# Kernel tuning notes

Hardware: AMD Instinct MI355X
Metric: run time of the kernel (lower is better)

The kernel has to match this reference:

```python
import jax, jax.numpy as jnp
import numpy as np

BN_EPS = 1e-5


def setup_inputs() -> dict:
    key = jax.random.key(0)
    ks = jax.random.split(key, 12)
    B, N, S, D1, D2 = 8, 8192, 2048, 128, 256
    C_in = D2 + D1  # 384
    mlp = [256, 128]
    inp = {
        "xyz1": jax.random.normal(ks[0], (B, 3, N), jnp.float32),
        "xyz2": jax.random.normal(ks[1], (B, 3, S), jnp.float32),
        "points1": jax.random.normal(ks[2], (B, D1, N), jnp.float32),
        "points2": jax.random.normal(ks[3], (B, D2, S), jnp.float32),
    }
    # conv0: in 384 -> 256, conv1: 256 -> 128 (1x1 Conv1d == per-point matmul)
    inp["w0"] = jax.random.normal(ks[4], (mlp[0], C_in), jnp.float32) * (1.0 / np.sqrt(C_in))
    inp["b0"] = jax.random.normal(ks[5], (mlp[0],), jnp.float32) * 0.01
    inp["g0"] = jnp.ones((mlp[0],), jnp.float32)
    inp["be0"] = jnp.zeros((mlp[0],), jnp.float32)
    inp["w1"] = jax.random.normal(ks[6], (mlp[1], mlp[0]), jnp.float32) * (1.0 / np.sqrt(mlp[0]))
    inp["b1"] = jax.random.normal(ks[7], (mlp[1],), jnp.float32) * 0.01
    inp["g1"] = jnp.ones((mlp[1],), jnp.float32)
    inp["be1"] = jnp.zeros((mlp[1],), jnp.float32)
    return inp


def _conv_bn_relu(x, w, b, g, be):
    # 1x1 Conv1d + BatchNorm1d (training-mode batch stats, biased var) + ReLU
    x = jnp.einsum("oc,bcn->bon", w, x) + b[None, :, None]
    m = jnp.mean(x, axis=(0, 2), keepdims=True)
    v = jnp.var(x, axis=(0, 2), keepdims=True)
    x = (x - m) * jax.lax.rsqrt(v + BN_EPS) * g[None, :, None] + be[None, :, None]
    return jax.nn.relu(x)


def reference(xyz1, xyz2, points1, points2, w0, b0, g0, be0, w1, b1, g1, be1):
    B, _, N = xyz1.shape
    S = xyz2.shape[2]
    src = jnp.transpose(xyz1, (0, 2, 1))  # [B,N,3]
    dst = jnp.transpose(xyz2, (0, 2, 1))  # [B,S,3]
    # squared pairwise distance [B,N,S]
    dist = (
        jnp.sum(src * src, axis=-1)[:, :, None]
        + jnp.sum(dst * dst, axis=-1)[:, None, :]
        - 2.0 * jnp.einsum("bnc,bsc->bns", src, dst)
    )
    # 3 nearest neighbors (smallest dist, sorted)
    neg_d, idx = jax.lax.top_k(-dist, 3)  # [B,N,3]
    d3 = -neg_d
    recip = 1.0 / (d3 + 1e-8)
    weight = recip / jnp.sum(recip, axis=-1, keepdims=True)  # [B,N,3]
    p2t = jnp.transpose(points2, (0, 2, 1))  # [B,S,D']
    gathered = jnp.take_along_axis(
        p2t, idx.reshape(B, N * 3)[:, :, None], axis=1
    ).reshape(B, N, 3, -1)  # [B,N,3,D']
    interp = jnp.einsum("bnkd,bnk->bdn", gathered, weight)  # [B,D',N]
    x = jnp.concatenate([interp, points1], axis=1)  # [B,D'+D,N]
    x = _conv_bn_relu(x, w0, b0, g0, be0)
    x = _conv_bn_relu(x, w1, b1, g1, be1)
    return x
```

## Files before the change

### kernel.cpp

```cpp
#include <hip/hip_runtime.h>
#include <hip/hip_bf16.h>

constexpr int kB = 8, kN = 8192, kS = 2048;
constexpr int kD1 = 128, kD2 = 256, kCin = 384, kM0 = 256, kM1 = 128;
constexpr float kEps = 1e-5f;
constexpr int kReps = 64;

typedef float f32x4 __attribute__((ext_vector_type(4)));
typedef short bf16x8 __attribute__((ext_vector_type(8)));
typedef unsigned short u16x4 __attribute__((ext_vector_type(4)));

__device__ inline unsigned short f2bf(float f) {
    __hip_bfloat16 h = __float2bfloat16(f);
    return *reinterpret_cast<unsigned short*>(&h);
}
__device__ inline float bf2f(unsigned short u) {
    unsigned int v = (unsigned int)u << 16;
    return *reinterpret_cast<float*>(&v);
}
__device__ inline unsigned uminu(unsigned a, unsigned b) { return a < b ? a : b; }
__device__ inline unsigned med3u(unsigned a, unsigned b, unsigned c) {
    unsigned d;
    asm("v_med3_u32 %0, %1, %2, %3" : "=v"(d) : "v"(a), "v"(b), "v"(c));
    return d;
}
#define INS4(K0, K1, K2, K3, X) do { unsigned _x = (X);          \
    K3 = med3u(_x, K2, K3);                                      \
    K2 = med3u(_x, K1, K2);                                      \
    K1 = med3u(_x, K0, K1);                                      \
    K0 = uminu(_x, K0); } while (0)

__global__ __launch_bounds__(256) void prep_kernel(
    const float* __restrict__ points2, float* __restrict__ p2t,
    const float* __restrict__ points1, unsigned short* __restrict__ xt,
    const float* __restrict__ xyz2, f32x4* __restrict__ spk,
    float* __restrict__ repl, float* __restrict__ smallstats,
    const float* __restrict__ w0, unsigned short* __restrict__ w0bf,
    const float* __restrict__ w1, unsigned short* __restrict__ w1bf)
{
    __shared__ float tl[64][69];
    const int bx = blockIdx.x;
    const int t = threadIdx.x;
    const int rlo = t >> 4, rhi = t & 15;
    if (bx < 1024) {
        const int b = bx >> 7, tile = bx & 127;
        const int s0 = (tile & 31) * 64, c0 = (tile >> 5) * 64;
#pragma unroll
        for (int r = 0; r < 4; ++r) {
            const int cl = rlo + r * 16;
            f32x4 v = *(const f32x4*)(points2 + ((size_t)(b * kD2 + c0 + cl)) * kS + s0 + rhi * 4);
#pragma unroll
            for (int j = 0; j < 4; ++j) tl[cl][rhi * 4 + j] = v[j];
        }
        __syncthreads();
#pragma unroll
        for (int r = 0; r < 4; ++r) {
            const int sl = rlo + r * 16;
            f32x4 v;
#pragma unroll
            for (int j = 0; j < 4; ++j) v[j] = tl[rhi * 4 + j][sl];
            *(f32x4*)(p2t + ((size_t)(b * kS + s0 + sl)) * kD2 + c0 + rhi * 4) = v;
        }
    } else if (bx < 3072) {
        const int idx = bx - 1024;
        const int b = idx >> 8, tile = idx & 255;
        const int n0 = (tile & 127) * 64, c0 = (tile >> 7) * 64;
#pragma unroll
        for (int r = 0; r < 4; ++r) {
            const int cl = rlo + r * 16;
            f32x4 v = *(const f32x4*)(points1 + ((size_t)(b * kD1 + c0 + cl)) * kN + n0 + rhi * 4);
#pragma unroll
            for (int j = 0; j < 4; ++j) tl[cl][rhi * 4 + j] = v[j];
        }
        __syncthreads();
#pragma unroll
        for (int r = 0; r < 4; ++r) {
            const int nl = rlo + r * 16;
            u16x4 u;
#pragma unroll
            for (int j = 0; j < 4; ++j) u[j] = f2bf(tl[rhi * 4 + j][nl]);
            *(u16x4*)(xt + ((size_t)(b * kN + n0 + nl)) * kCin + 256 + c0 + rhi * 4) = u;
        }
    } else if (bx < 3080) {
        const int b = bx - 3072;
        const float* x2 = xyz2 + b * 3 * kS;
        for (int s = t; s < kS; s += 256) {
            float sx = x2[s], sy = x2[kS + s], sz = x2[2 * kS + s];
            f32x4 q = {sx, sy, sz, fmaf(sx, sx, fmaf(sy, sy, sz * sz))};
            spk[b * kS + s] = q;
        }
        for (int i = b * 6144 + t; i < (b + 1) * 6144; i += 256) repl[i] = 0.f;
        if (b == 0) for (int i = t; i < 772; i += 256) smallstats[i] = 0.f;
    } else if (bx < 3096) {
        const int base = (bx - 3080) * 256 + t;
        for (int c = base; c < kM0 * kCin / 4; c += 4096) {
            f32x4 v = *(const f32x4*)(w0 + (size_t)c * 4);
            u16x4 u = {f2bf(v[0]), f2bf(v[1]), f2bf(v[2]), f2bf(v[3])};
            *(u16x4*)(w0bf + (size_t)c * 4) = u;
        }
    } else {
        const int base = (bx - 3096) * 256 + t;
        for (int c = base; c < kM1 * kM0 / 4; c += 2048) {
            f32x4 v = *(const f32x4*)(w1 + (size_t)c * 4);
            u16x4 u = {f2bf(v[0]), f2bf(v[1]), f2bf(v[2]), f2bf(v[3])};
            *(u16x4*)(w1bf + (size_t)c * 4) = u;
        }
    }
}

__global__ __launch_bounds__(256) void knn_interp_kernel(
    const float* __restrict__ xyz1, const f32x4* __restrict__ spk,
    const float* __restrict__ p2t, unsigned short* __restrict__ xt,
    int* __restrict__ flaglist, int* __restrict__ flagcount)
{
    __shared__ f32x4 sp[kS];
    const int bb = blockIdx.x >> 7;
    const int nblk = (blockIdx.x & 127) << 6;
    const int t = threadIdx.x;
    for (int s = t; s < kS; s += 256) sp[s] = spk[bb * kS + s];
    __syncthreads();
    const int q = t >> 2, c = t & 3;
    const int nq = nblk + q;
    const float* x1 = xyz1 + bb * 3 * kN;
    const float px = x1[nq], py = x1[kN + nq], pz = x1[2 * kN + nq];
    const float ax = -2.f * px, ay = -2.f * py, az = -2.f * pz;
    const float pp = fmaf(px, px, fmaf(py, py, pz * pz));

    unsigned k0 = 0xFFFFFFFFu, k1 = 0xFFFFFFFFu, k2 = 0xFFFFFFFFu, k3 = 0xFFFFFFFFu;
#pragma unroll 8
    for (int i = 0; i < 512; ++i) {
        const f32x4 qv = sp[4 * i + c];
        const float e = fmaxf(fmaf(ax, qv[0], fmaf(ay, qv[1], fmaf(az, qv[2], qv[3] + pp))), 0.f);
        const unsigned x = (__float_as_uint(e) & 0xFFFFF800u) | (unsigned)(4 * i + c);
        INS4(k0, k1, k2, k3, x);
    }
#pragma unroll
    for (int off = 1; off <= 2; off <<= 1) {
        const unsigned m0 = __shfl_xor(k0, off), m1 = __shfl_xor(k1, off);
        const unsigned m2 = __shfl_xor(k2, off), m3 = __shfl_xor(k3, off);
        INS4(k0, k1, k2, k3, m0); INS4(k0, k1, k2, k3, m1);
        INS4(k0, k1, k2, k3, m2); INS4(k0, k1, k2, k3, m3);
    }

    bool flag = false;
    float w0f = 0.f, w1f = 0.f, w2f = 0.f;
    int i0 = (int)(k0 & 2047u), i1 = (int)(k1 & 2047u), i2 = (int)(k2 & 2047u);
    if (c == 0) {
        const float v2t = __uint_as_float(k2 & 0xFFFFF800u);
        const float v3t = __uint_as_float(k3 & 0xFFFFF800u);
        flag = (v3t - v2t) <= fmaf(v3t, 1e-3f, 2.5e-4f);
        const double dpx = (double)px, dpy = (double)py, dpz = (double)pz;
        const f32x4 s0 = sp[i0], s1 = sp[i1], s2 = sp[i2];
        double d0 = (dpx - s0[0]) * (dpx - s0[0]) + (dpy - s0[1]) * (dpy - s0[1]) + (dpz - s0[2]) * (dpz - s0[2]);
        double d1 = (dpx - s1[0]) * (dpx - s1[0]) + (dpy - s1[1]) * (dpy - s1[1]) + (dpz - s1[2]) * (dpz - s1[2]);
        double d2 = (dpx - s2[0]) * (dpx - s2[0]) + (dpy - s2[1]) * (dpy - s2[1]) + (dpz - s2[2]) * (dpz - s2[2]);
        if (d1 < d0 || (d1 == d0 && i1 < i0)) { double td = d0; d0 = d1; d1 = td; int ti = i0; i0 = i1; i1 = ti; }
        if (d2 < d1 || (d2 == d1 && i2 < i1)) { double td = d1; d1 = d2; d2 = td; int ti = i1; i1 = i2; i2 = ti; }
        if (d1 < d0 || (d1 == d0 && i1 < i0)) { double td = d0; d0 = d1; d1 = td; int ti = i0; i0 = i1; i1 = ti; }
        const double r0 = 1.0 / (d0 + 1e-8), r1 = 1.0 / (d1 + 1e-8), r2 = 1.0 / (d2 + 1e-8);
        const double rs = 1.0 / (r0 + r1 + r2);
        w0f = (float)(r0 * rs); w1f = (float)(r1 * rs); w2f = (float)(r2 * rs);
    }
    const int src = (t & 63) & ~3;
    w0f = __shfl(w0f, src); w1f = __shfl(w1f, src); w2f = __shfl(w2f, src);
    i0 = __shfl(i0, src); i1 = __shfl(i1, src); i2 = __shfl(i2, src);

    {
        const unsigned long long bal = __ballot(flag);
        if (bal) {
            const int l = t & 63;
            int base = 0;
            if (l == 0) base = atomicAdd(flagcount, __popcll(bal));
            base = __shfl(base, 0);
            if (flag) {
                const int pre = __popcll(bal & ((1ull << l) - 1ull));
                flaglist[base + pre] = (bb << 13) | nq;
            }
        }
    }

    const f32x4* row0 = (const f32x4*)(p2t + ((size_t)(bb * kS) + i0) * kD2);
    const f32x4* row1 = (const f32x4*)(p2t + ((size_t)(bb * kS) + i1) * kD2);
    const f32x4* row2 = (const f32x4*)(p2t + ((size_t)(bb * kS) + i2) * kD2);
    unsigned short* dst = xt + ((size_t)(bb * kN) + nq) * kCin;
#pragma unroll 4
    for (int j = 0; j < 16; ++j) {
        const int ch = c + 4 * j;
        f32x4 v = w0f * row0[ch] + w1f * row1[ch] + w2f * row2[ch];
        u16x4 u = {f2bf(v[0]), f2bf(v[1]), f2bf(v[2]), f2bf(v[3])};
        *(u16x4*)(dst + ch * 4) = u;
    }
}
#undef INS4

__global__ __launch_bounds__(256) void knn_fallback_kernel(
    const float* __restrict__ xyz1, const f32x4* __restrict__ spk,
    const float* __restrict__ p2t, unsigned short* __restrict__ xt,
    const int* __restrict__ flaglist, const int* __restrict__ flagcount)
{
    const int cnt = *flagcount;
    const int t = threadIdx.x;
    const int w = t >> 6, l = t & 63;
    for (int idx = blockIdx.x * 4 + w; idx < cnt; idx += gridDim.x * 4) {
        const int code = flaglist[idx];
        const int b = code >> 13, n = code & 8191;
        const float* x1 = xyz1 + b * 3 * kN;
        const double px = (double)x1[n], py = (double)x1[kN + n], pz = (double)x1[2 * kN + n];
        double d0 = 1e300, d1 = 1e300, d2 = 1e300;
        int i0 = 0, i1 = 0, i2 = 0;
        for (int s = l; s < kS; s += 64) {
            const f32x4 q = spk[b * kS + s];
            const double ex = px - (double)q[0], ey = py - (double)q[1], ez = pz - (double)q[2];
            const double d = ex * ex + ey * ey + ez * ez;
            if (d < d2) {
                if (d < d1) {
                    if (d < d0) { d2 = d1; i2 = i1; d1 = d0; i1 = i0; d0 = d; i0 = s; }
                    else        { d2 = d1; i2 = i1; d1 = d;  i1 = s; }
                } else          { d2 = d;  i2 = s; }
            }
        }
#pragma unroll
        for (int off = 1; off < 64; off <<= 1) {
            double pd0 = __shfl_xor(d0, off), pd1 = __shfl_xor(d1, off), pd2 = __shfl_xor(d2, off);
            int pi0 = __shfl_xor(i0, off), pi1 = __shfl_xor(i1, off), pi2 = __shfl_xor(i2, off);
#pragma unroll
            for (int m = 0; m < 3; ++m) {
                const double pd = (m == 0) ? pd0 : (m == 1) ? pd1 : pd2;
                const int pi = (m == 0) ? pi0 : (m == 1) ? pi1 : pi2;
                if (pd < d2 || (pd == d2 && pi < i2)) {
                    if (pd < d1 || (pd == d1 && pi < i1)) {
                        if (pd < d0 || (pd == d0 && pi < i0)) {
                            d2 = d1; i2 = i1; d1 = d0; i1 = i0; d0 = pd; i0 = pi;
                        } else { d2 = d1; i2 = i1; d1 = pd; i1 = pi; }
                    } else { d2 = pd; i2 = pi; }
                }
            }
        }
        const double r0 = 1.0 / (d0 + 1e-8), r1 = 1.0 / (d1 + 1e-8), r2 = 1.0 / (d2 + 1e-8);
        const double rs = 1.0 / (r0 + r1 + r2);
        const float w0f = (float)(r0 * rs), w1f = (float)(r1 * rs), w2f = (float)(r2 * rs);
        const f32x4* row0 = (const f32x4*)(p2t + ((size_t)(b * kS) + i0) * kD2);
        const f32x4* row1 = (const f32x4*)(p2t + ((size_t)(b * kS) + i1) * kD2);
        const f32x4* row2 = (const f32x4*)(p2t + ((size_t)(b * kS) + i2) * kD2);
        const f32x4 v = w0f * row0[l] + w1f * row1[l] + w2f * row2[l];
        u16x4 u = {f2bf(v[0]), f2bf(v[1]), f2bf(v[2]), f2bf(v[3])};
        *(u16x4*)(xt + ((size_t)(b * kN) + n) * kCin + l * 4) = u;
    }
}

__device__ inline int swz(int row, int ks) {
    return row * 32 + ((ks ^ ((row >> 1) & 3)) << 3);
}

template <int K, int MTOT, bool BNRELU, int OUTMODE, bool STATS>
__global__ __launch_bounds__(256) void gemm_bn_kernel(
    const unsigned short* __restrict__ Wbf, const unsigned short* __restrict__ X,
    const float* __restrict__ scale, const float* __restrict__ shift,
    unsigned short* __restrict__ Yb, float* __restrict__ Yf,
    float* __restrict__ repl)
{
    constexpr int BM = 128, BN = 64;
    __shared__ unsigned short Al[2][BM * 32], Bl[2][BN * 32];
    __shared__ float ssum[BM], ssq[BM];
    __shared__ float s_sc[K], s_sh[K];
    const int t = threadIdx.x;
    const int bn = blockIdx.x * BN, bo = blockIdx.y * BM, b = blockIdx.z;
    const int l = t & 63, w = t >> 6;
    const int wm = (w >> 1) * 64, wn = (w & 1) * 32;
    const int lrow = l & 15, lks = l >> 4;

    if constexpr (BNRELU) {
        if (t < K) { s_sc[t] = scale[t]; s_sh[t] = shift[t]; }
    }
    if constexpr (STATS) {
        if (t < BM) { ssum[t] = 0.f; ssq[t] = 0.f; }
    }
    __syncthreads();

    const int mA0 = t >> 2, ksA = t & 3;
    const int mA1 = mA0 + 64;
    const int nB = t >> 2, ksB = t & 3;
    bf16x8 rA0, rA1, rB;

    auto load_tile = [&](int k0) {
        rA0 = *(const bf16x8*)(Wbf + (size_t)(bo + mA0) * K + k0 + ksA * 8);
        rA1 = *(const bf16x8*)(Wbf + (size_t)(bo + mA1) * K + k0 + ksA * 8);
        rB  = *(const bf16x8*)(X + ((size_t)(b * kN) + bn + nB) * K + k0 + ksB * 8);
    };
    auto write_tile = [&](int buf, int k0) {
        *(bf16x8*)(&Al[buf][0] + swz(mA0, ksA)) = rA0;
        *(bf16x8*)(&Al[buf][0] + swz(mA1, ksA)) = rA1;
        bf16x8 v = rB;
        if constexpr (BNRELU) {
#pragma unroll
            for (int j = 0; j < 8; ++j) {
                const int ch = k0 + ksB * 8 + j;
                float f = fmaxf(fmaf(bf2f((unsigned short)v[j]), s_sc[ch], s_sh[ch]), 0.f);
                v[j] = (short)f2bf(f);
            }
        }
        *(bf16x8*)(&Bl[buf][0] + swz(nB, ksB)) = v;
    };

    f32x4 acc[4][2] = {};
    load_tile(0);
    write_tile(0, 0);
    __syncthreads();
    int cur = 0;
    for (int k0 = 32; k0 <= K; k0 += 32) {
        if (k0 < K) load_tile(k0);
        bf16x8 af[4], bfr[2];
#pragma unroll
        for (int f = 0; f < 4; ++f) af[f]  = *(const bf16x8*)(&Al[cur][0] + swz(wm + f * 16 + lrow, lks));
#pragma unroll
        for (int f = 0; f < 2; ++f) bfr[f] = *(const bf16x8*)(&Bl[cur][0] + swz(wn + f * 16 + lrow, lks));
#pragma unroll
        for (int mi = 0; mi < 4; ++mi)
#pragma unroll
            for (int ni = 0; ni < 2; ++ni)
                acc[mi][ni] = __builtin_amdgcn_mfma_f32_16x16x32_bf16(af[mi], bfr[ni], acc[mi][ni], 0, 0, 0);
        if (k0 < K) { write_tile(cur ^ 1, k0); cur ^= 1; }
        __syncthreads();
    }

    if constexpr (STATS) {
#pragma unroll
        for (int mi = 0; mi < 4; ++mi) {
#pragma unroll
            for (int r = 0; r < 4; ++r) {
                float ps = 0.f, pq = 0.f;
#pragma unroll
                for (int ni = 0; ni < 2; ++ni) { float v = acc[mi][ni][r]; ps += v; pq += v * v; }
#pragma unroll
                for (int off = 1; off < 16; off <<= 1) { ps += __shfl_xor(ps, off); pq += __shfl_xor(pq, off); }
                if (lrow == 0) {
                    const int m = wm + mi * 16 + lks * 4 + r;
                    atomicAdd(&ssum[m], ps); atomicAdd(&ssq[m], pq);
                }
            }
        }
    }

    if constexpr (OUTMODE == 0) {
#pragma unroll
        for (int mi = 0; mi < 4; ++mi)
#pragma unroll
            for (int ni = 0; ni < 2; ++ni) {
                const int m = bo + wm + mi * 16 + lks * 4;
                const int n = bn + wn + ni * 16 + lrow;
                u16x4 u = {f2bf(acc[mi][ni][0]), f2bf(acc[mi][ni][1]),
                           f2bf(acc[mi][ni][2]), f2bf(acc[mi][ni][3])};
                *(u16x4*)(Yb + ((size_t)(b * kN) + n) * MTOT + m) = u;
            }
    } else {
#pragma unroll
        for (int mi = 0; mi < 4; ++mi)
#pragma unroll
            for (int ni = 0; ni < 2; ++ni) {
                const int n = bn + wn + ni * 16 + lrow;
#pragma unroll
                for (int r = 0; r < 4; ++r) {
                    const int m = bo + wm + mi * 16 + lks * 4 + r;
                    Yf[((size_t)(b * MTOT) + m) * kN + n] = acc[mi][ni][r];
                }
            }
    }
    if constexpr (STATS) {
        __syncthreads();
        if (t < BM) {
            const int rep = (blockIdx.x + blockIdx.z * 8) & (kReps - 1);
            float* rp = repl + (size_t)rep * (2 * MTOT);
            atomicAdd(&rp[bo + t], ssum[t]);
            atomicAdd(&rp[MTOT + bo + t], ssq[t]);
        }
    }
}

__global__ void bn_finalize_kernel(const float* __restrict__ repl,
                                   const float* __restrict__ g, const float* __restrict__ be,
                                   float* __restrict__ scale, float* __restrict__ shift, int M)
{
    const int t = threadIdx.x;
    if (t < M) {
        float s = 0.f, q = 0.f;
#pragma unroll 8
        for (int r = 0; r < kReps; ++r) {
            s += repl[(size_t)r * 2 * M + t];
            q += repl[(size_t)r * 2 * M + M + t];
        }
        const float invn = 1.0f / 65536.0f;
        const float mean = s * invn;
        const float var = q * invn - mean * mean;
        const float sc = g[t] * rsqrtf(var + kEps);
        scale[t] = sc;
        shift[t] = fmaf(-mean, sc, be[t]);
    }
}

__global__ __launch_bounds__(256) void bn_relu_out_kernel(
    float* __restrict__ out, const float* __restrict__ scale, const float* __restrict__ shift)
{
    const int total = kB * kM1 * kN / 4;
    for (int idx = blockIdx.x * blockDim.x + threadIdx.x; idx < total;
         idx += gridDim.x * blockDim.x) {
        const int p = (idx >> 11) & 127;
        const float sc = scale[p], sh = shift[p];
        f32x4 v = ((f32x4*)out)[idx];
#pragma unroll
        for (int j = 0; j < 4; ++j) v[j] = fmaxf(fmaf(v[j], sc, sh), 0.f);
        ((f32x4*)out)[idx] = v;
    }
}

extern "C" void kernel_launch(void* const* d_in, const int* in_sizes, int n_in,
                              void* d_out, int out_size, void* d_ws, size_t ws_size,
                              hipStream_t stream)
{
    const float* xyz1    = (const float*)d_in[0];
    const float* xyz2    = (const float*)d_in[1];
    const float* points1 = (const float*)d_in[2];
    const float* points2 = (const float*)d_in[3];
    const float* w0      = (const float*)d_in[4];
    const float* g0      = (const float*)d_in[6];
    const float* be0     = (const float*)d_in[7];
    const float* w1      = (const float*)d_in[8];
    const float* g1      = (const float*)d_in[10];
    const float* be1     = (const float*)d_in[11];
    float* out = (float*)d_out;

    char* ws = (char*)d_ws;
    unsigned short* xt  = (unsigned short*)ws;
    float* p2t          = (float*)(ws + (size_t)50331648);
    unsigned short* y0t = (unsigned short*)(ws + (size_t)67108864);
    float* repl0        = (float*)(ws + (size_t)100663296);
    float* repl1        = (float*)(ws + (size_t)100794368);
    float* smallstats   = (float*)(ws + (size_t)100859904);
    f32x4* spk          = (f32x4*)(ws + (size_t)104857600);
    int*  flaglist      = (int*)(ws + (size_t)105906176);
    unsigned short* w0bf = (unsigned short*)(ws + (size_t)106954752);
    unsigned short* w1bf = (unsigned short*)(ws + (size_t)107151360);
    float* scale0 = smallstats,       *shift0 = smallstats + 256;
    float* scale1 = smallstats + 512, *shift1 = smallstats + 640;
    int*  flagcount = (int*)(smallstats + 768);

    prep_kernel<<<3104, 256, 0, stream>>>(points2, p2t, points1, xt, xyz2, spk,
                                          repl0, smallstats, w0, w0bf, w1, w1bf);
    knn_interp_kernel<<<1024, 256, 0, stream>>>(xyz1, spk, p2t, xt, flaglist, flagcount);
    knn_fallback_kernel<<<1024, 256, 0, stream>>>(xyz1, spk, p2t, xt, flaglist, flagcount);
    gemm_bn_kernel<kCin, kM0, false, 0, true><<<dim3(128, 2, 8), 256, 0, stream>>>(
        w0bf, xt, nullptr, nullptr, y0t, nullptr, repl0);
    bn_finalize_kernel<<<1, 256, 0, stream>>>(repl0, g0, be0, scale0, shift0, 256);
    gemm_bn_kernel<kM0, kM1, true, 1, true><<<dim3(128, 1, 8), 256, 0, stream>>>(
        w1bf, y0t, scale0, shift0, nullptr, out, repl1);
    bn_finalize_kernel<<<1, 128, 0, stream>>>(repl1, g1, be1, scale1, shift1, 128);
    bn_relu_out_kernel<<<2048, 256, 0, stream>>>(out, scale1, shift1);
}
```

Before: 160.0 us.

## Register-block 4 query points per thread in KNN scan to reuse LDS loads

Reworks the KNN top-4 scan so each thread handles 4 query points over a 16-way split of the source points, instead of 1 point over a 4-way split. Each LDS load of a source point is now reused across 4 queries, cutting LDS traffic per distance evaluation. The price is a longer shuffle-merge tree (4 xor stages instead of 2) and more registers. Results are passed to the gather phase through shared memory plus an extra barrier rather than lane shuffles.

```diff
diff --git a/kernel.cpp b/kernel.cpp
--- a/kernel.cpp
+++ b/kernel.cpp
@@ -114,42 +114,64 @@
     int* __restrict__ flaglist, int* __restrict__ flagcount)
 {
     __shared__ f32x4 sp[kS];
+    __shared__ float gw[64][3];
+    __shared__ int   gi[64][3];
     const int bb = blockIdx.x >> 7;
     const int nblk = (blockIdx.x & 127) << 6;
     const int t = threadIdx.x;
     for (int s = t; s < kS; s += 256) sp[s] = spk[bb * kS + s];
     __syncthreads();
-    const int q = t >> 2, c = t & 3;
-    const int nq = nblk + q;
+    const int grp = t >> 4, l16 = t & 15;
+    const int q0 = nblk + grp * 4;
     const float* x1 = xyz1 + bb * 3 * kN;
-    const float px = x1[nq], py = x1[kN + nq], pz = x1[2 * kN + nq];
-    const float ax = -2.f * px, ay = -2.f * py, az = -2.f * pz;
-    const float pp = fmaf(px, px, fmaf(py, py, pz * pz));
-
-    unsigned k0 = 0xFFFFFFFFu, k1 = 0xFFFFFFFFu, k2 = 0xFFFFFFFFu, k3 = 0xFFFFFFFFu;
-#pragma unroll 8
-    for (int i = 0; i < 512; ++i) {
-        const f32x4 qv = sp[4 * i + c];
-        const float e = fmaxf(fmaf(ax, qv[0], fmaf(ay, qv[1], fmaf(az, qv[2], qv[3] + pp))), 0.f);
-        const unsigned x = (__float_as_uint(e) & 0xFFFFF800u) | (unsigned)(4 * i + c);
-        INS4(k0, k1, k2, k3, x);
-    }
-#pragma unroll
-    for (int off = 1; off <= 2; off <<= 1) {
-        const unsigned m0 = __shfl_xor(k0, off), m1 = __shfl_xor(k1, off);
-        const unsigned m2 = __shfl_xor(k2, off), m3 = __shfl_xor(k3, off);
-        INS4(k0, k1, k2, k3, m0); INS4(k0, k1, k2, k3, m1);
-        INS4(k0, k1, k2, k3, m2); INS4(k0, k1, k2, k3, m3);
+    float ax[4], ay[4], az[4], ppv[4];
+#pragma unroll
+    for (int j = 0; j < 4; ++j) {
+        const float px = x1[q0 + j], py = x1[kN + q0 + j], pz = x1[2 * kN + q0 + j];
+        ax[j] = -2.f * px; ay[j] = -2.f * py; az[j] = -2.f * pz;
+        ppv[j] = fmaf(px, px, fmaf(py, py, pz * pz));
+    }
+
+    unsigned ka[4], kb[4], kc[4], kd[4];
+#pragma unroll
+    for (int j = 0; j < 4; ++j) { ka[j] = kb[j] = kc[j] = kd[j] = 0xFFFFFFFFu; }
+#pragma unroll 4
+    for (int i = 0; i < 128; ++i) {
+        const int s = l16 + 16 * i;
+        const f32x4 qv = sp[s];
+#pragma unroll
+        for (int j = 0; j < 4; ++j) {
+            const float e = fmaxf(fmaf(ax[j], qv[0], fmaf(ay[j], qv[1],
+                                fmaf(az[j], qv[2], qv[3] + ppv[j]))), 0.f);
+            const unsigned x = (__float_as_uint(e) & 0xFFFFF800u) | (unsigned)s;
+            INS4(ka[j], kb[j], kc[j], kd[j], x);
+        }
+    }
+#pragma unroll
+    for (int off = 1; off <= 8; off <<= 1) {
+#pragma unroll
+        for (int j = 0; j < 4; ++j) {
+            const unsigned m0 = __shfl_xor(ka[j], off), m1 = __shfl_xor(kb[j], off);
+            const unsigned m2 = __shfl_xor(kc[j], off), m3 = __shfl_xor(kd[j], off);
+            INS4(ka[j], kb[j], kc[j], kd[j], m0); INS4(ka[j], kb[j], kc[j], kd[j], m1);
+            INS4(ka[j], kb[j], kc[j], kd[j], m2); INS4(ka[j], kb[j], kc[j], kd[j], m3);
+        }
     }
 
     bool flag = false;
-    float w0f = 0.f, w1f = 0.f, w2f = 0.f;
-    int i0 = (int)(k0 & 2047u), i1 = (int)(k1 & 2047u), i2 = (int)(k2 & 2047u);
-    if (c == 0) {
-        const float v2t = __uint_as_float(k2 & 0xFFFFF800u);
-        const float v3t = __uint_as_float(k3 & 0xFFFFF800u);
+    if (l16 < 4) {
+        const unsigned c0 = l16 == 0 ? ka[0] : l16 == 1 ? ka[1] : l16 == 2 ? ka[2] : ka[3];
+        const unsigned c1 = l16 == 0 ? kb[0] : l16 == 1 ? kb[1] : l16 == 2 ? kb[2] : kb[3];
+        const unsigned c2 = l16 == 0 ? kc[0] : l16 == 1 ? kc[1] : l16 == 2 ? kc[2] : kc[3];
+        const unsigned c3 = l16 == 0 ? kd[0] : l16 == 1 ? kd[1] : l16 == 2 ? kd[2] : kd[3];
+        const float axx = l16 == 0 ? ax[0] : l16 == 1 ? ax[1] : l16 == 2 ? ax[2] : ax[3];
+        const float ayy = l16 == 0 ? ay[0] : l16 == 1 ? ay[1] : l16 == 2 ? ay[2] : ay[3];
+        const float azz = l16 == 0 ? az[0] : l16 == 1 ? az[1] : l16 == 2 ? az[2] : az[3];
+        int i0 = (int)(c0 & 2047u), i1 = (int)(c1 & 2047u), i2 = (int)(c2 & 2047u);
+        const float v2t = __uint_as_float(c2 & 0xFFFFF800u);
+        const float v3t = __uint_as_float(c3 & 0xFFFFF800u);
         flag = (v3t - v2t) <= fmaf(v3t, 1e-3f, 2.5e-4f);
-        const double dpx = (double)px, dpy = (double)py, dpz = (double)pz;
+        const double dpx = -0.5 * (double)axx, dpy = -0.5 * (double)ayy, dpz = -0.5 * (double)azz;
         const f32x4 s0 = sp[i0], s1 = sp[i1], s2 = sp[i2];
         double d0 = (dpx - s0[0]) * (dpx - s0[0]) + (dpy - s0[1]) * (dpy - s0[1]) + (dpz - s0[2]) * (dpz - s0[2]);
         double d1 = (dpx - s1[0]) * (dpx - s1[0]) + (dpy - s1[1]) * (dpy - s1[1]) + (dpz - s1[2]) * (dpz - s1[2]);
@@ -159,12 +181,10 @@
         if (d1 < d0 || (d1 == d0 && i1 < i0)) { double td = d0; d0 = d1; d1 = td; int ti = i0; i0 = i1; i1 = ti; }
         const double r0 = 1.0 / (d0 + 1e-8), r1 = 1.0 / (d1 + 1e-8), r2 = 1.0 / (d2 + 1e-8);
         const double rs = 1.0 / (r0 + r1 + r2);
-        w0f = (float)(r0 * rs); w1f = (float)(r1 * rs); w2f = (float)(r2 * rs);
-    }
-    const int src = (t & 63) & ~3;
-    w0f = __shfl(w0f, src); w1f = __shfl(w1f, src); w2f = __shfl(w2f, src);
-    i0 = __shfl(i0, src); i1 = __shfl(i1, src); i2 = __shfl(i2, src);
-
+        const int gq = grp * 4 + l16;
+        gw[gq][0] = (float)(r0 * rs); gw[gq][1] = (float)(r1 * rs); gw[gq][2] = (float)(r2 * rs);
+        gi[gq][0] = i0; gi[gq][1] = i1; gi[gq][2] = i2;
+    }
     {
         const unsigned long long bal = __ballot(flag);
         if (bal) {
@@ -174,18 +194,22 @@
             base = __shfl(base, 0);
             if (flag) {
                 const int pre = __popcll(bal & ((1ull << l) - 1ull));
-                flaglist[base + pre] = (bb << 13) | nq;
-            }
-        }
-    }
-
-    const f32x4* row0 = (const f32x4*)(p2t + ((size_t)(bb * kS) + i0) * kD2);
-    const f32x4* row1 = (const f32x4*)(p2t + ((size_t)(bb * kS) + i1) * kD2);
-    const f32x4* row2 = (const f32x4*)(p2t + ((size_t)(bb * kS) + i2) * kD2);
+                flaglist[base + pre] = (bb << 13) | (nblk + grp * 4 + l16);
+            }
+        }
+    }
+    __syncthreads();
+
+    const int q = t >> 2, c4 = t & 3;
+    const int nq = nblk + q;
+    const float w0f = gw[q][0], w1f = gw[q][1], w2f = gw[q][2];
+    const f32x4* row0 = (const f32x4*)(p2t + ((size_t)(bb * kS) + gi[q][0]) * kD2);
+    const f32x4* row1 = (const f32x4*)(p2t + ((size_t)(bb * kS) + gi[q][1]) * kD2);
+    const f32x4* row2 = (const f32x4*)(p2t + ((size_t)(bb * kS) + gi[q][2]) * kD2);
     unsigned short* dst = xt + ((size_t)(bb * kN) + nq) * kCin;
 #pragma unroll 4
     for (int j = 0; j < 16; ++j) {
-        const int ch = c + 4 * j;
+        const int ch = c4 + 4 * j;
         f32x4 v = w0f * row0[ch] + w1f * row1[ch] + w2f * row2[ch];
         u16x4 u = {f2bf(v[0]), f2bf(v[1]), f2bf(v[2]), f2bf(v[3])};
         *(u16x4*)(dst + ch * 4) = u;
```

New measurement: 162.0 us. Within noise of the previous version (+1.3%).
